# Performance work log

Hardware: AMD Instinct MI355X
Metric: run time of the kernel (lower is better)

## Reference

```python
import jax, jax.numpy as jnp
import numpy as np

B, T, D, H, E, NHEADS = 32, 512, 64, 128, 256, 8  # E = 2*H (bidirectional concat)


def setup_inputs() -> dict:
    key = jax.random.key(0)
    ks = jax.random.split(key, 20)
    s = 0.05

    def gl(k, shape):
        return jax.random.normal(k, shape, dtype=jnp.float32) * s

    inp = {}
    inp["x"] = jax.random.normal(ks[0], (B, T, D), dtype=jnp.float32)
    inp["mask"] = (jax.random.uniform(ks[1], (B, T, D)) > 0.3).astype(jnp.float32)
    # Fused GRU-D gate params per direction: rows ordered [r; z; n]
    inp["fwd_Wi"] = gl(ks[2], (3 * H, D));  inp["fwd_bi"] = gl(ks[3], (3 * H,))
    inp["fwd_Wh"] = gl(ks[4], (3 * H, H));  inp["fwd_bh"] = gl(ks[5], (3 * H,))
    inp["bwd_Wi"] = gl(ks[6], (3 * H, D));  inp["bwd_bi"] = gl(ks[7], (3 * H,))
    inp["bwd_Wh"] = gl(ks[8], (3 * H, H));  inp["bwd_bh"] = gl(ks[9], (3 * H,))
    # nn.MultiheadAttention params (in_proj packs q,k,v)
    inp["attn_w_in"] = gl(ks[10], (3 * E, E)); inp["attn_b_in"] = gl(ks[11], (3 * E,))
    inp["attn_w_out"] = gl(ks[12], (E, E));    inp["attn_b_out"] = gl(ks[13], (E,))
    # output projection 2H -> input_dim
    inp["out_w"] = gl(ks[14], (D, E));         inp["out_b"] = gl(ks[15], (D,))
    return inp


def gru_scan(xm, Wi, bi, Wh, bh):
    """GRU over time. xm: [T, B, D_in] (already mask-multiplied). Returns [T, B, H]."""
    Wh_rz, Wh_n = Wh[: 2 * H], Wh[2 * H :]
    bh_rz, bh_n = bh[: 2 * H], bh[2 * H :]

    def step(h, xt):
        gi = xt @ Wi.T + bi                      # [B, 3H]
        i_r, i_z, i_n = jnp.split(gi, 3, axis=-1)
        g_rz = h @ Wh_rz.T + bh_rz               # [B, 2H]
        r = jax.nn.sigmoid(i_r + g_rz[:, :H])
        z = jax.nn.sigmoid(i_z + g_rz[:, H:])
        n = jnp.tanh(i_n + (r * h) @ Wh_n.T + bh_n)
        h_new = (1.0 - z) * n + z * h
        return h_new, h_new

    h0 = jnp.zeros((xm.shape[1], H), dtype=xm.dtype)
    _, hs = jax.lax.scan(step, h0, xm)
    return hs


def mha(xt, Win, bin_, Wout, bout):
    """torch nn.MultiheadAttention (seq-first, self-attn, no mask). xt: [T, B, E]."""
    Tn, Bn, En = xt.shape
    hd = En // NHEADS
    qkv = xt @ Win.T + bin_                      # [T, B, 3E]
    q, k, v = jnp.split(qkv, 3, axis=-1)
    q = q.reshape(Tn, Bn, NHEADS, hd) * (1.0 / np.sqrt(hd))
    k = k.reshape(Tn, Bn, NHEADS, hd)
    v = v.reshape(Tn, Bn, NHEADS, hd)
    scores = jnp.einsum("tbhd,sbhd->bhts", q, k)   # [B, H, T, T]
    attn = jax.nn.softmax(scores, axis=-1)
    o = jnp.einsum("bhts,sbhd->tbhd", attn, v).reshape(Tn, Bn, En)
    return o @ Wout.T + bout


def reference(x, mask, fwd_Wi, fwd_bi, fwd_Wh, fwd_bh,
              bwd_Wi, bwd_bi, bwd_Wh, bwd_bh,
              attn_w_in, attn_b_in, attn_w_out, attn_b_out,
              out_w, out_b):
    xm = (x * mask).transpose(1, 0, 2)           # [T, B, D]
    hf = gru_scan(xm, fwd_Wi, fwd_bi, fwd_Wh, fwd_bh)                 # forward in time
    hb = gru_scan(xm[::-1], bwd_Wi, bwd_bi, bwd_Wh, bwd_bh)[::-1]     # backward in time
    hc = jnp.concatenate([hf, hb], axis=-1)      # [T, B, 2H]
    hc = mha(hc, attn_w_in, attn_b_in, attn_w_out, attn_b_out)
    imputed = (hc @ out_w.T + out_b).transpose(1, 0, 2)  # [B, T, D]
    output = x * mask + imputed * (1.0 - mask)
    return (output, imputed)
```

## Files before the change

kernel.cpp:

```cpp
#include <hip/hip_runtime.h>

#define TT 512
#define BB 32
#define DD 64
#define HH 128
#define EE 256
#define NR 16384

typedef _Float16 h2v __attribute__((ext_vector_type(2)));
typedef short bf16x8 __attribute__((ext_vector_type(8)));
typedef float f32x4 __attribute__((ext_vector_type(4)));

static __device__ __forceinline__ float bflo(unsigned u){ return __uint_as_float(u << 16); }
static __device__ __forceinline__ float bfhi(unsigned u){ return __uint_as_float(u & 0xFFFF0000u); }
static __device__ __forceinline__ unsigned short f2bf(float x){
  unsigned u = __float_as_uint(x);
  return (unsigned short)((u + 0x7FFFu + ((u >> 16) & 1u)) >> 16);
}
static __device__ __forceinline__ unsigned packbf(float a, float b){
  return (unsigned)f2bf(a) | ((unsigned)f2bf(b) << 16);
}
static __device__ __forceinline__ float sigmoidf_(float x){
  return 1.0f / (1.0f + __expf(-x));
}
static __device__ __forceinline__ float tanhf_(float x){
  float e = __expf(2.0f * x);
  return 1.0f - 2.0f / (e + 1.0f);
}
static __device__ __forceinline__ unsigned packh2(float a, float b){
  h2v v; v.x = (_Float16)a; v.y = (_Float16)b;
  return __builtin_bit_cast(unsigned, v);
}
#define BCH(u) __builtin_bit_cast(h2v, (u))
#define DOT2(a, b, c) __builtin_amdgcn_fdot2((a), (b), (c), false)
#define LGKM_BARRIER() asm volatile("s_waitcnt lgkmcnt(0)\n\ts_barrier" ::: "memory")

__global__ __launch_bounds__(256) void gi_mfma_kernel(
    const float* __restrict__ x, const float* __restrict__ mask,
    const float* __restrict__ WiF, const float* __restrict__ biF,
    const float* __restrict__ WiB, const float* __restrict__ biB,
    float* __restrict__ gi)
{
  __shared__ unsigned short As[64*72];
  __shared__ unsigned short Ws[64*72];
  int tid = threadIdx.x;
  int r0 = blockIdx.x * 64;
  int lane = tid & 63;
  int w = tid >> 6;
  int lr = lane & 15, lk = lane >> 4;

#pragma unroll
  for (int it = 0; it < 4; ++it) {
    int l = tid + it*256;
    int row = l >> 4, kq = l & 15;
    int r = r0 + row; int t = r >> 5, b = r & 31;
    const float* xr = x + ((size_t)b*TT + t)*DD + kq*4;
    const float* mr = mask + ((size_t)b*TT + t)*DD + kq*4;
    float4 xv = *(const float4*)xr;
    float4 mv = *(const float4*)mr;
    unsigned* dst = (unsigned*)&As[row*72 + kq*4];
    dst[0] = packbf(xv.x*mv.x, xv.y*mv.y);
    dst[1] = packbf(xv.z*mv.z, xv.w*mv.w);
  }

  for (int ch = 0; ch < 12; ++ch) {
    int c0 = ch * 64;
    __syncthreads();
#pragma unroll
    for (int it = 0; it < 4; ++it) {
      int l = tid + it*256;
      int col = l >> 4, kq = l & 15;
      int c = c0 + col;
      const float* wr = (c < 384 ? WiF + (size_t)c*64 : WiB + (size_t)(c-384)*64) + kq*4;
      float4 v = *(const float4*)wr;
      unsigned* dst = (unsigned*)&Ws[col*72 + kq*4];
      dst[0] = packbf(v.x, v.y);
      dst[1] = packbf(v.z, v.w);
    }
    __syncthreads();

    const unsigned short* arow = &As[(w*16 + lr)*72 + lk*8];
    f32x4 acc[4];
#pragma unroll
    for (int ct = 0; ct < 4; ++ct) {
      int cg = c0 + ct*16 + lr;
      float bv = (cg < 384) ? biF[cg] : biB[cg - 384];
      acc[ct][0] = bv; acc[ct][1] = bv; acc[ct][2] = bv; acc[ct][3] = bv;
    }
#pragma unroll
    for (int ks = 0; ks < 2; ++ks) {
      bf16x8 a = *(const bf16x8*)(arow + ks*32);
#pragma unroll
      for (int ct = 0; ct < 4; ++ct) {
        bf16x8 wv = *(const bf16x8*)&Ws[(ct*16 + lr)*72 + lk*8 + ks*32];
        acc[ct] = __builtin_amdgcn_mfma_f32_16x16x32_bf16(a, wv, acc[ct], 0, 0, 0);
      }
    }
#pragma unroll
    for (int ct = 0; ct < 4; ++ct) {
#pragma unroll
      for (int j = 0; j < 4; ++j) {
        int row = r0 + w*16 + lk*4 + j;
        gi[(size_t)row*768 + c0 + ct*16 + lr] = acc[ct][j];
      }
    }
  }
}

__global__ __launch_bounds__(256)
__attribute__((amdgpu_waves_per_eu(1, 1)))
void scan_kernel(
    const float* __restrict__ gi,
    const float* __restrict__ WhF, const float* __restrict__ bhF,
    const float* __restrict__ WhB, const float* __restrict__ bhB,
    float* __restrict__ hc)
{
  int dir = blockIdx.x >> 5;
  int b = blockIdx.x & 31;
  const float* Wh = dir ? WhB : WhF;
  const float* bh = dir ? bhB : bhF;
  int tid = threadIdx.x;
  int j2 = tid >> 1, h2 = tid & 1;

  __shared__ __align__(16) float h_s[128];
  __shared__ __align__(16) unsigned hs16[68];
  __shared__ __align__(16) unsigned rh16[76];
  __shared__ float z_s[128];

  const float* wp1 = Wh + (size_t)tid * 128;
#define LDA(n) unsigned A##n = packh2(wp1[2*(n)], wp1[2*(n)+1]);
  LDA(0) LDA(1) LDA(2) LDA(3) LDA(4) LDA(5) LDA(6) LDA(7)
  LDA(8) LDA(9) LDA(10) LDA(11) LDA(12) LDA(13) LDA(14) LDA(15)
  LDA(16) LDA(17) LDA(18) LDA(19) LDA(20) LDA(21) LDA(22) LDA(23)
  LDA(24) LDA(25) LDA(26) LDA(27) LDA(28) LDA(29) LDA(30) LDA(31)
  LDA(32) LDA(33) LDA(34) LDA(35) LDA(36) LDA(37) LDA(38) LDA(39)
  LDA(40) LDA(41) LDA(42) LDA(43) LDA(44) LDA(45) LDA(46) LDA(47)
  LDA(48) LDA(49) LDA(50) LDA(51) LDA(52) LDA(53) LDA(54) LDA(55)
  LDA(56) LDA(57) LDA(58) LDA(59) LDA(60) LDA(61) LDA(62) LDA(63)
#undef LDA
  const float* wp2 = Wh + (size_t)(256 + j2) * 128 + h2 * 64;
#define LDB(n) unsigned B##n = packh2(wp2[2*(n)], wp2[2*(n)+1]);
  LDB(0) LDB(1) LDB(2) LDB(3) LDB(4) LDB(5) LDB(6) LDB(7)
  LDB(8) LDB(9) LDB(10) LDB(11) LDB(12) LDB(13) LDB(14) LDB(15)
  LDB(16) LDB(17) LDB(18) LDB(19) LDB(20) LDB(21) LDB(22) LDB(23)
  LDB(24) LDB(25) LDB(26) LDB(27) LDB(28) LDB(29) LDB(30) LDB(31)
#undef LDB

  float bh1 = bh[tid];
  float bh2 = bh[256 + j2];

  if (tid < 128) h_s[tid] = 0.0f;
  if (tid < 68)  hs16[tid] = 0u;
  __syncthreads();

  size_t row0 = dir ? ((size_t)(TT-1)*BB + b) : (size_t)b;
  const float* grow = gi + row0 * 768 + dir * 384;
  long dstep = (dir ? -(long)BB : (long)BB) * 768;
  float gi1v = grow[tid];
  float gi2v = grow[256 + j2];

  for (int s = 0; s < TT; s++) {
#define PIN8(a,b_,c,d,e,f,g,hh) asm volatile("" : "+v"(a), "+v"(b_), "+v"(c), "+v"(d), "+v"(e), "+v"(f), "+v"(g), "+v"(hh));
    PIN8(A0,A1,A2,A3,A4,A5,A6,A7)
    PIN8(A8,A9,A10,A11,A12,A13,A14,A15)
    PIN8(A16,A17,A18,A19,A20,A21,A22,A23)
    PIN8(A24,A25,A26,A27,A28,A29,A30,A31)
    PIN8(A32,A33,A34,A35,A36,A37,A38,A39)
    PIN8(A40,A41,A42,A43,A44,A45,A46,A47)
    PIN8(A48,A49,A50,A51,A52,A53,A54,A55)
    PIN8(A56,A57,A58,A59,A60,A61,A62,A63)
    PIN8(B0,B1,B2,B3,B4,B5,B6,B7)
    PIN8(B8,B9,B10,B11,B12,B13,B14,B15)
    PIN8(B16,B17,B18,B19,B20,B21,B22,B23)
    PIN8(B24,B25,B26,B27,B28,B29,B30,B31)
#undef PIN8

    const float* gnext = grow + dstep;
    float gi1n = 0.f, gi2n = 0.f;
    if (s + 1 < TT) { gi1n = gnext[tid]; gi2n = gnext[256 + j2]; }

    float hold = h_s[tid & 127];

    const unsigned* hp0 = hs16;
    const unsigned* hp1 = hs16 + 36;
    float ya = 0.f, yb = 0.f, yc = 0.f, yd = 0.f;
#define S1(n, base, w0, w1, w2, w3) { uint4 hv = *(const uint4*)((base) + 4*(n)); \
    ya = DOT2(BCH(w0), BCH(hv.x), ya); yb = DOT2(BCH(w1), BCH(hv.y), yb); \
    yc = DOT2(BCH(w2), BCH(hv.z), yc); yd = DOT2(BCH(w3), BCH(hv.w), yd); }
    S1(0, hp0, A0,A1,A2,A3)     S1(1, hp0, A4,A5,A6,A7)
    S1(2, hp0, A8,A9,A10,A11)   S1(3, hp0, A12,A13,A14,A15)
    S1(4, hp0, A16,A17,A18,A19) S1(5, hp0, A20,A21,A22,A23)
    S1(6, hp0, A24,A25,A26,A27) S1(7, hp0, A28,A29,A30,A31)
    S1(0, hp1, A32,A33,A34,A35) S1(1, hp1, A36,A37,A38,A39)
    S1(2, hp1, A40,A41,A42,A43) S1(3, hp1, A44,A45,A46,A47)
    S1(4, hp1, A48,A49,A50,A51) S1(5, hp1, A52,A53,A54,A55)
    S1(6, hp1, A56,A57,A58,A59) S1(7, hp1, A60,A61,A62,A63)
#undef S1
    float y = (ya + yb) + (yc + yd);
    float sg = sigmoidf_(gi1v + y + bh1);
    float rhv = sg * hold;
    float rhp = __shfl_xor(rhv, 1);
    if (tid < 128) {
      if ((tid & 1) == 0) {
        int pi = tid >> 1;
        rh16[(pi & 15) + 20 * (pi >> 4)] = packh2(rhv, rhp);
      }
    } else {
      z_s[tid - 128] = sg;
    }
    LGKM_BARRIER();

    const unsigned* rp0 = rh16 + h2 * 40;
    const unsigned* rp1 = rp0 + 20;
    float ca = 0.f, cb = 0.f, cc = 0.f, cd = 0.f;
#define S2(n, base, w0, w1, w2, w3) { uint4 rv = *(const uint4*)((base) + 4*(n)); \
    ca = DOT2(BCH(w0), BCH(rv.x), ca); cb = DOT2(BCH(w1), BCH(rv.y), cb); \
    cc = DOT2(BCH(w2), BCH(rv.z), cc); cd = DOT2(BCH(w3), BCH(rv.w), cd); }
    S2(0, rp0, B0,B1,B2,B3)     S2(1, rp0, B4,B5,B6,B7)
    S2(2, rp0, B8,B9,B10,B11)   S2(3, rp0, B12,B13,B14,B15)
    S2(0, rp1, B16,B17,B18,B19) S2(1, rp1, B20,B21,B22,B23)
    S2(2, rp1, B24,B25,B26,B27) S2(3, rp1, B28,B29,B30,B31)
#undef S2
    float y2 = (ca + cb) + (cc + cd);
    y2 += __shfl_xor(y2, 1);
    float nn = tanhf_(gi2v + y2 + bh2);
    float zv = z_s[j2];
    float hv_ = h_s[j2];
    float hn = nn + zv * (hv_ - nn);
    float hnp = __shfl_xor(hn, 2);
    if (h2 == 0) {
      h_s[j2] = hn;
      int t = dir ? (TT - 1 - s) : s;
      hc[((size_t)t * BB + b) * EE + dir * HH + j2] = hn;
    }
    if ((tid & 3) == 0) {
      int pi = tid >> 2;
      hs16[(pi & 31) + 36 * (j2 >> 6)] = packh2(hn, hnp);
    }
    LGKM_BARRIER();
    gi1v = gi1n; gi2v = gi2n;
    grow = gnext;
  }
}

__global__ __launch_bounds__(256) void mfma_gemm_kernel(
    const float* __restrict__ A, const float* __restrict__ W,
    const float* __restrict__ bias, float* __restrict__ C,
    int N)
{
  __shared__ unsigned short As[64*264];
  __shared__ unsigned short Ws[64*264];
  int tid = threadIdx.x;
  int r0 = blockIdx.x * 64;
  int lane = tid & 63;
  int w = tid >> 6;
  int lr = lane & 15;
  int lk = lane >> 4;

#pragma unroll
  for (int it = 0; it < 16; ++it) {
    int l = tid + it*256;
    int row = l >> 6, kq = l & 63;
    float4 v = *(const float4*)(A + (size_t)(r0+row)*256 + kq*4);
    unsigned* dst = (unsigned*)&As[row*264 + kq*4];
    dst[0] = packbf(v.x, v.y);
    dst[1] = packbf(v.z, v.w);
  }

  const unsigned short* arow = &As[(w*16 + lr)*264 + lk*8];
  const unsigned short* wrow0 = &Ws[(0*16 + lr)*264 + lk*8];
  const unsigned short* wrow1 = &Ws[(1*16 + lr)*264 + lk*8];
  const unsigned short* wrow2 = &Ws[(2*16 + lr)*264 + lk*8];
  const unsigned short* wrow3 = &Ws[(3*16 + lr)*264 + lk*8];

  int nChunks = N >> 6;
  for (int ch = 0; ch < nChunks; ++ch) {
    int c0 = ch << 6;
    __syncthreads();
#pragma unroll
    for (int it = 0; it < 16; ++it) {
      int l = tid + it*256;
      int row = l >> 6, kq = l & 63;
      float4 v = *(const float4*)(W + (size_t)(c0+row)*256 + kq*4);
      unsigned* dst = (unsigned*)&Ws[row*264 + kq*4];
      dst[0] = packbf(v.x, v.y);
      dst[1] = packbf(v.z, v.w);
    }
    __syncthreads();

    float b0 = bias[c0 + lr], b1 = bias[c0 + 16 + lr];
    float b2 = bias[c0 + 32 + lr], b3 = bias[c0 + 48 + lr];
    f32x4 acc0 = {b0, b0, b0, b0};
    f32x4 acc1 = {b1, b1, b1, b1};
    f32x4 acc2 = {b2, b2, b2, b2};
    f32x4 acc3 = {b3, b3, b3, b3};

#pragma unroll
    for (int ks = 0; ks < 8; ++ks) {
      bf16x8 a  = *(const bf16x8*)(arow  + ks*32);
      bf16x8 q0 = *(const bf16x8*)(wrow0 + ks*32);
      bf16x8 q1 = *(const bf16x8*)(wrow1 + ks*32);
      bf16x8 q2 = *(const bf16x8*)(wrow2 + ks*32);
      bf16x8 q3 = *(const bf16x8*)(wrow3 + ks*32);
      acc0 = __builtin_amdgcn_mfma_f32_16x16x32_bf16(a, q0, acc0, 0, 0, 0);
      acc1 = __builtin_amdgcn_mfma_f32_16x16x32_bf16(a, q1, acc1, 0, 0, 0);
      acc2 = __builtin_amdgcn_mfma_f32_16x16x32_bf16(a, q2, acc2, 0, 0, 0);
      acc3 = __builtin_amdgcn_mfma_f32_16x16x32_bf16(a, q3, acc3, 0, 0, 0);
    }

#pragma unroll
    for (int j = 0; j < 4; ++j) {
      int row = r0 + w*16 + lk*4 + j;
      float* cp = C + (size_t)row * N + c0 + lr;
      cp[0]  = acc0[j];
      cp[16] = acc1[j];
      cp[32] = acc2[j];
      cp[48] = acc3[j];
    }
  }
}

__global__ __launch_bounds__(256, 1) void attn_mfma_kernel(
    const float* __restrict__ qkv, float* __restrict__ obuf)
{
  int b = blockIdx.x >> 3, h = blockIdx.x & 7;
  int tid = threadIdx.x;
  int lane = tid & 63;
  int w = tid >> 6;
  int lr = lane & 15, lk = lane >> 4;

  __shared__ unsigned short Ks[512*40];
  __shared__ unsigned short Vt[32*520];
  __shared__ unsigned short Sb[64*520];
  __shared__ unsigned short Qs[64*40];

  for (int l = tid; l < 4096; l += 256) {
    int s = l >> 3, dq = l & 7;
    const float* kr = qkv + ((size_t)s*BB + b)*768 + 256 + h*32 + dq*4;
    float4 kv = *(const float4*)kr;
    unsigned* kd = (unsigned*)&Ks[s*40 + dq*4];
    kd[0] = packbf(kv.x, kv.y);
    kd[1] = packbf(kv.z, kv.w);
    float4 vv = *(const float4*)(kr + 256);
    int sp = ((s & 15) << 5) + (s >> 4);
    Vt[(dq*4+0)*520 + sp] = f2bf(vv.x);
    Vt[(dq*4+1)*520 + sp] = f2bf(vv.y);
    Vt[(dq*4+2)*520 + sp] = f2bf(vv.z);
    Vt[(dq*4+3)*520 + sp] = f2bf(vv.w);
  }
  __syncthreads();

  const float SCL = 0.17677669529663687f;

  for (int p = 0; p < 8; ++p) {
    int q0 = p*64 + w*16;
#pragma unroll
    for (int i = 0; i < 2; ++i) {
      int l = lane + i*64;
      int row = l >> 3, dq = l & 7;
      const float* qr = qkv + ((size_t)(q0+row)*BB + b)*768 + h*32 + dq*4;
      float4 qv = *(const float4*)qr;
      unsigned* qd = (unsigned*)&Qs[(w*16+row)*40 + dq*4];
      qd[0] = packbf(qv.x*SCL, qv.y*SCL);
      qd[1] = packbf(qv.z*SCL, qv.w*SCL);
    }
    bf16x8 a = *(const bf16x8*)&Qs[(w*16+lr)*40 + lk*8];
    f32x4 st[32];
#pragma unroll
    for (int t = 0; t < 32; ++t) {
      bf16x8 kb = *(const bf16x8*)&Ks[(t*16+lr)*40 + lk*8];
      f32x4 z = {0.f, 0.f, 0.f, 0.f};
      st[t] = __builtin_amdgcn_mfma_f32_16x16x32_bf16(a, kb, z, 0, 0, 0);
    }
    float inv[4];
#pragma unroll
    for (int j = 0; j < 4; ++j) {
      float m = -3e38f;
#pragma unroll
      for (int t = 0; t < 32; ++t) m = fmaxf(m, st[t][j]);
      m = fmaxf(m, __shfl_xor(m, 1));
      m = fmaxf(m, __shfl_xor(m, 2));
      m = fmaxf(m, __shfl_xor(m, 4));
      m = fmaxf(m, __shfl_xor(m, 8));
      float sum = 0.f;
#pragma unroll
      for (int t = 0; t < 32; ++t) { float e = __expf(st[t][j] - m); st[t][j] = e; sum += e; }
      sum += __shfl_xor(sum, 1);
      sum += __shfl_xor(sum, 2);
      sum += __shfl_xor(sum, 4);
      sum += __shfl_xor(sum, 8);
      inv[j] = 1.0f / sum;
    }
#pragma unroll
    for (int j = 0; j < 4; ++j) {
      unsigned pk[16];
#pragma unroll
      for (int i = 0; i < 16; ++i)
        pk[i] = packbf(st[2*i][j]*inv[j], st[2*i+1][j]*inv[j]);
      uint4* dst = (uint4*)&Sb[(w*16 + lk*4 + j)*520 + lr*32];
      dst[0] = make_uint4(pk[0], pk[1], pk[2], pk[3]);
      dst[1] = make_uint4(pk[4], pk[5], pk[6], pk[7]);
      dst[2] = make_uint4(pk[8], pk[9], pk[10], pk[11]);
      dst[3] = make_uint4(pk[12], pk[13], pk[14], pk[15]);
    }
    f32x4 o0 = {0.f,0.f,0.f,0.f}, o1 = {0.f,0.f,0.f,0.f};
#pragma unroll
    for (int kt = 0; kt < 16; ++kt) {
      bf16x8 pa = *(const bf16x8*)&Sb[(w*16 + lr)*520 + kt*32 + lk*8];
      bf16x8 v0 = *(const bf16x8*)&Vt[(lr)*520 + kt*32 + lk*8];
      bf16x8 v1 = *(const bf16x8*)&Vt[(16 + lr)*520 + kt*32 + lk*8];
      o0 = __builtin_amdgcn_mfma_f32_16x16x32_bf16(pa, v0, o0, 0, 0, 0);
      o1 = __builtin_amdgcn_mfma_f32_16x16x32_bf16(pa, v1, o1, 0, 0, 0);
    }
#pragma unroll
    for (int j = 0; j < 4; ++j) {
      int q = q0 + lk*4 + j;
      float* op = obuf + ((size_t)q*BB + b)*EE + h*32;
      op[lr]      = o0[j];
      op[16 + lr] = o1[j];
    }
  }
}

__global__ __launch_bounds__(256) void fuse_w_kernel(
    const float* __restrict__ aWout, const float* __restrict__ about,
    const float* __restrict__ oW, const float* __restrict__ ob,
    float* __restrict__ Wf, float* __restrict__ bf)
{
  int g = blockIdx.x;
  int k = threadIdx.x;
  const float* owr = oW + (size_t)g * 256;
  float acc = 0.f;
  for (int j = 0; j < 256; ++j)
    acc += owr[j] * aWout[(size_t)j * 256 + k];
  Wf[(size_t)g * 256 + k] = acc;
  if (k == 0) {
    float a = ob[g];
    for (int j = 0; j < 256; ++j) a += owr[j] * about[j];
    bf[g] = a;
  }
}

__global__ __launch_bounds__(256) void final_kernel(
    const float* __restrict__ A,
    const float* __restrict__ W,
    const float* __restrict__ bias,
    const float* __restrict__ x, const float* __restrict__ mask,
    float* __restrict__ out)
{
  __shared__ float As[64*260];
  __shared__ unsigned Ws[64*130];
  int tid = threadIdx.x;
  int ty = tid >> 4, tx = tid & 15;
  int r0 = blockIdx.x * 64;

  for (int l = tid; l < 4096; l += 256) {
    int row = l >> 6, kq = l & 63;
    float4 v = *(const float4*)(A + (size_t)(r0 + row)*256 + kq*4);
    *(float4*)&As[row*260 + kq*4] = v;
  }
  for (int l = tid; l < 4096; l += 256) {
    int c = l >> 6, kq = l & 63;
    float4 v = *(const float4*)(W + (size_t)c*256 + kq*4);
    uint2 p; p.x = packbf(v.x, v.y); p.y = packbf(v.z, v.w);
    *(uint2*)&Ws[c*130 + kq*2] = p;
  }
  __syncthreads();

  float acc[4][4];
#pragma unroll
  for (int rj = 0; rj < 4; rj++)
#pragma unroll
    for (int cj = 0; cj < 4; cj++)
      acc[rj][cj] = bias[tx + 16*cj];

#pragma unroll 2
  for (int kq = 0; kq < 64; kq++) {
    float4 av[4];
#pragma unroll
    for (int rj = 0; rj < 4; rj++)
      av[rj] = *(const float4*)&As[(ty*4+rj)*260 + 4*kq];
#pragma unroll
    for (int cj = 0; cj < 4; cj++) {
      uint2 w2 = *(const uint2*)&Ws[(tx + 16*cj)*130 + 2*kq];
      float w0 = bflo(w2.x), w1 = bfhi(w2.x);
      float w2f = bflo(w2.y), w3 = bfhi(w2.y);
#pragma unroll
      for (int rj = 0; rj < 4; rj++)
        acc[rj][cj] += av[rj].x*w0 + av[rj].y*w1 + av[rj].z*w2f + av[rj].w*w3;
    }
  }

#pragma unroll
  for (int rj = 0; rj < 4; rj++) {
    int r = r0 + ty*4 + rj;
    int t = r >> 5, b = r & 31;
    size_t base = ((size_t)b * TT + t) * DD;
#pragma unroll
    for (int cj = 0; cj < 4; cj++) {
      int c = tx + 16*cj;
      float imp = acc[rj][cj];
      float xv = x[base + c], mv = mask[base + c];
      out[base + c] = xv*mv + imp*(1.0f - mv);
      out[(size_t)1048576 + base + c] = imp;
    }
  }
}

extern "C" void kernel_launch(void* const* d_in, const int* in_sizes, int n_in,
                              void* d_out, int out_size, void* d_ws, size_t ws_size,
                              hipStream_t stream) {
  const float* x     = (const float*)d_in[0];
  const float* mask  = (const float*)d_in[1];
  const float* fWi   = (const float*)d_in[2];
  const float* fbi   = (const float*)d_in[3];
  const float* fWh   = (const float*)d_in[4];
  const float* fbh   = (const float*)d_in[5];
  const float* bWi   = (const float*)d_in[6];
  const float* bbi   = (const float*)d_in[7];
  const float* bWh   = (const float*)d_in[8];
  const float* bbh   = (const float*)d_in[9];
  const float* aWin  = (const float*)d_in[10];
  const float* abin  = (const float*)d_in[11];
  const float* aWout = (const float*)d_in[12];
  const float* about = (const float*)d_in[13];
  const float* oW    = (const float*)d_in[14];
  const float* ob    = (const float*)d_in[15];
  float* out = (float*)d_out;
  float* ws  = (float*)d_ws;

  float* gi   = ws;
  float* hc   = ws + 12582912;
  float* qkv  = ws;
  float* obuf = ws + 12582912;
  float* Wf   = ws;
  float* bf   = ws + 16384;

  gi_mfma_kernel<<<256, 256, 0, stream>>>(x, mask, fWi, fbi, bWi, bbi, gi);
  scan_kernel<<<64, 256, 0, stream>>>(gi, fWh, fbh, bWh, bbh, hc);
  mfma_gemm_kernel<<<256, 256, 0, stream>>>(hc, aWin, abin, qkv, 768);
  attn_mfma_kernel<<<256, 256, 0, stream>>>(qkv, obuf);
  fuse_w_kernel<<<64, 256, 0, stream>>>(aWout, about, oW, ob, Wf, bf);
  final_kernel<<<256, 256, 0, stream>>>(obuf, Wf, bf, x, mask, out);
}
```

Measured before the change: 599.9 us.

## Batch GRU recurrence across 16 sequences per block using bf16 MFMA

The recurrent scan now has each block handle 16 batch rows for one direction and computes the hidden-state matmuls with bf16 MFMA instructions, using register-resident weight fragments. This replaces the previous design of one block per sequence using fp16 dot2 instructions. The grid shrinks from 64 blocks to 4, so far fewer CUs are used, but each step does 16x the work per block on matrix cores. Precision moves from fp16 to bf16 for the recurrent state, which may increase accumulated error over the 512 steps.

```diff
diff --git a/kernel.cpp b/kernel.cpp
--- a/kernel.cpp
+++ b/kernel.cpp
@@ -7,7 +7,6 @@
 #define EE 256
 #define NR 16384
 
-typedef _Float16 h2v __attribute__((ext_vector_type(2)));
 typedef short bf16x8 __attribute__((ext_vector_type(8)));
 typedef float f32x4 __attribute__((ext_vector_type(4)));
 
@@ -27,13 +26,16 @@
   float e = __expf(2.0f * x);
   return 1.0f - 2.0f / (e + 1.0f);
 }
-static __device__ __forceinline__ unsigned packh2(float a, float b){
-  h2v v; v.x = (_Float16)a; v.y = (_Float16)b;
-  return __builtin_bit_cast(unsigned, v);
-}
-#define BCH(u) __builtin_bit_cast(h2v, (u))
-#define DOT2(a, b, c) __builtin_amdgcn_fdot2((a), (b), (c), false)
 #define LGKM_BARRIER() asm volatile("s_waitcnt lgkmcnt(0)\n\ts_barrier" ::: "memory")
+
+static __device__ __forceinline__ bf16x8 ldwfrag(const float* p){
+  float4 u = *(const float4*)p;
+  float4 v = *(const float4*)(p + 4);
+  uint4 q;
+  q.x = packbf(u.x, u.y); q.y = packbf(u.z, u.w);
+  q.z = packbf(v.x, v.y); q.w = packbf(v.z, v.w);
+  return __builtin_bit_cast(bf16x8, q);
+}
 
 __global__ __launch_bounds__(256) void gi_mfma_kernel(
     const float* __restrict__ x, const float* __restrict__ mask,
@@ -109,136 +111,165 @@
 
 __global__ __launch_bounds__(256)
 __attribute__((amdgpu_waves_per_eu(1, 1)))
-void scan_kernel(
+void scan_mfma_kernel(
     const float* __restrict__ gi,
     const float* __restrict__ WhF, const float* __restrict__ bhF,
     const float* __restrict__ WhB, const float* __restrict__ bhB,
     float* __restrict__ hc)
 {
-  int dir = blockIdx.x >> 5;
-  int b = blockIdx.x & 31;
+  int dir = blockIdx.x >> 1;
+  int bhalf = blockIdx.x & 1;
   const float* Wh = dir ? WhB : WhF;
   const float* bh = dir ? bhB : bhF;
   int tid = threadIdx.x;
-  int j2 = tid >> 1, h2 = tid & 1;
-
-  __shared__ __align__(16) float h_s[128];
-  __shared__ __align__(16) unsigned hs16[68];
-  __shared__ __align__(16) unsigned rh16[76];
-  __shared__ float z_s[128];
-
-  const float* wp1 = Wh + (size_t)tid * 128;
-#define LDA(n) unsigned A##n = packh2(wp1[2*(n)], wp1[2*(n)+1]);
-  LDA(0) LDA(1) LDA(2) LDA(3) LDA(4) LDA(5) LDA(6) LDA(7)
-  LDA(8) LDA(9) LDA(10) LDA(11) LDA(12) LDA(13) LDA(14) LDA(15)
-  LDA(16) LDA(17) LDA(18) LDA(19) LDA(20) LDA(21) LDA(22) LDA(23)
-  LDA(24) LDA(25) LDA(26) LDA(27) LDA(28) LDA(29) LDA(30) LDA(31)
-  LDA(32) LDA(33) LDA(34) LDA(35) LDA(36) LDA(37) LDA(38) LDA(39)
-  LDA(40) LDA(41) LDA(42) LDA(43) LDA(44) LDA(45) LDA(46) LDA(47)
-  LDA(48) LDA(49) LDA(50) LDA(51) LDA(52) LDA(53) LDA(54) LDA(55)
-  LDA(56) LDA(57) LDA(58) LDA(59) LDA(60) LDA(61) LDA(62) LDA(63)
-#undef LDA
-  const float* wp2 = Wh + (size_t)(256 + j2) * 128 + h2 * 64;
-#define LDB(n) unsigned B##n = packh2(wp2[2*(n)], wp2[2*(n)+1]);
-  LDB(0) LDB(1) LDB(2) LDB(3) LDB(4) LDB(5) LDB(6) LDB(7)
-  LDB(8) LDB(9) LDB(10) LDB(11) LDB(12) LDB(13) LDB(14) LDB(15)
-  LDB(16) LDB(17) LDB(18) LDB(19) LDB(20) LDB(21) LDB(22) LDB(23)
-  LDB(24) LDB(25) LDB(26) LDB(27) LDB(28) LDB(29) LDB(30) LDB(31)
-#undef LDB
-
-  float bh1 = bh[tid];
-  float bh2 = bh[256 + j2];
-
-  if (tid < 128) h_s[tid] = 0.0f;
-  if (tid < 68)  hs16[tid] = 0u;
+  int lane = tid & 63;
+  int w = tid >> 6;
+  int lr = lane & 15, lk = lane >> 4;
+
+  __shared__ unsigned short h16[16*136];
+  __shared__ unsigned short rh16[16*136];
+  __shared__ float hf[16*132];
+  __shared__ float zf[16*132];
+
+  bf16x8 WB1[4][4];
+#pragma unroll
+  for (int ct = 0; ct < 4; ++ct)
+#pragma unroll
+    for (int ks = 0; ks < 4; ++ks)
+      WB1[ct][ks] = ldwfrag(Wh + (size_t)((w*4+ct)*16 + lr)*128 + ks*32 + lk*8);
+  bf16x8 WB2[2][4];
+#pragma unroll
+  for (int ti = 0; ti < 2; ++ti)
+#pragma unroll
+    for (int ks = 0; ks < 4; ++ks)
+      WB2[ti][ks] = ldwfrag(Wh + (size_t)(256 + w*32 + ti*16 + lr)*128 + ks*32 + lk*8);
+
+  float bh1[4], bh2[2];
+#pragma unroll
+  for (int ct = 0; ct < 4; ++ct) bh1[ct] = bh[(w*4+ct)*16 + lr];
+#pragma unroll
+  for (int ti = 0; ti < 2; ++ti) bh2[ti] = bh[256 + w*32 + ti*16 + lr];
+
+  for (int l = tid; l < 16*136; l += 256) { h16[l] = 0; rh16[l] = 0; }
+  for (int l = tid; l < 16*132; l += 256) { hf[l] = 0.0f; zf[l] = 0.0f; }
   __syncthreads();
 
-  size_t row0 = dir ? ((size_t)(TT-1)*BB + b) : (size_t)b;
-  const float* grow = gi + row0 * 768 + dir * 384;
   long dstep = (dir ? -(long)BB : (long)BB) * 768;
-  float gi1v = grow[tid];
-  float gi2v = grow[256 + j2];
-
-  for (int s = 0; s < TT; s++) {
-#define PIN8(a,b_,c,d,e,f,g,hh) asm volatile("" : "+v"(a), "+v"(b_), "+v"(c), "+v"(d), "+v"(e), "+v"(f), "+v"(g), "+v"(hh));
-    PIN8(A0,A1,A2,A3,A4,A5,A6,A7)
-    PIN8(A8,A9,A10,A11,A12,A13,A14,A15)
-    PIN8(A16,A17,A18,A19,A20,A21,A22,A23)
-    PIN8(A24,A25,A26,A27,A28,A29,A30,A31)
-    PIN8(A32,A33,A34,A35,A36,A37,A38,A39)
-    PIN8(A40,A41,A42,A43,A44,A45,A46,A47)
-    PIN8(A48,A49,A50,A51,A52,A53,A54,A55)
-    PIN8(A56,A57,A58,A59,A60,A61,A62,A63)
-    PIN8(B0,B1,B2,B3,B4,B5,B6,B7)
-    PIN8(B8,B9,B10,B11,B12,B13,B14,B15)
-    PIN8(B16,B17,B18,B19,B20,B21,B22,B23)
-    PIN8(B24,B25,B26,B27,B28,B29,B30,B31)
-#undef PIN8
-
+  int t0_ = dir ? (TT-1) : 0;
+  const float* grow = gi + (size_t)(t0_*BB + bhalf*16) * 768 + dir*384;
+
+  float g1[4][4], g2[2][4];
+#pragma unroll
+  for (int ct = 0; ct < 4; ++ct)
+#pragma unroll
+    for (int j = 0; j < 4; ++j)
+      g1[ct][j] = grow[(size_t)(lk*4+j)*768 + (w*4+ct)*16 + lr];
+#pragma unroll
+  for (int ti = 0; ti < 2; ++ti)
+#pragma unroll
+    for (int j = 0; j < 4; ++j)
+      g2[ti][j] = grow[(size_t)(lk*4+j)*768 + 256 + w*32 + ti*16 + lr];
+
+  for (int s = 0; s < TT; ++s) {
+    int t = dir ? (TT - 1 - s) : s;
     const float* gnext = grow + dstep;
-    float gi1n = 0.f, gi2n = 0.f;
-    if (s + 1 < TT) { gi1n = gnext[tid]; gi2n = gnext[256 + j2]; }
-
-    float hold = h_s[tid & 127];
-
-    const unsigned* hp0 = hs16;
-    const unsigned* hp1 = hs16 + 36;
-    float ya = 0.f, yb = 0.f, yc = 0.f, yd = 0.f;
-#define S1(n, base, w0, w1, w2, w3) { uint4 hv = *(const uint4*)((base) + 4*(n)); \
-    ya = DOT2(BCH(w0), BCH(hv.x), ya); yb = DOT2(BCH(w1), BCH(hv.y), yb); \
-    yc = DOT2(BCH(w2), BCH(hv.z), yc); yd = DOT2(BCH(w3), BCH(hv.w), yd); }
-    S1(0, hp0, A0,A1,A2,A3)     S1(1, hp0, A4,A5,A6,A7)
-    S1(2, hp0, A8,A9,A10,A11)   S1(3, hp0, A12,A13,A14,A15)
-    S1(4, hp0, A16,A17,A18,A19) S1(5, hp0, A20,A21,A22,A23)
-    S1(6, hp0, A24,A25,A26,A27) S1(7, hp0, A28,A29,A30,A31)
-    S1(0, hp1, A32,A33,A34,A35) S1(1, hp1, A36,A37,A38,A39)
-    S1(2, hp1, A40,A41,A42,A43) S1(3, hp1, A44,A45,A46,A47)
-    S1(4, hp1, A48,A49,A50,A51) S1(5, hp1, A52,A53,A54,A55)
-    S1(6, hp1, A56,A57,A58,A59) S1(7, hp1, A60,A61,A62,A63)
-#undef S1
-    float y = (ya + yb) + (yc + yd);
-    float sg = sigmoidf_(gi1v + y + bh1);
-    float rhv = sg * hold;
-    float rhp = __shfl_xor(rhv, 1);
-    if (tid < 128) {
-      if ((tid & 1) == 0) {
-        int pi = tid >> 1;
-        rh16[(pi & 15) + 20 * (pi >> 4)] = packh2(rhv, rhp);
+
+    float g1n[4][4], g2n[2][4];
+    if (s + 1 < TT) {
+#pragma unroll
+      for (int ct = 0; ct < 4; ++ct)
+#pragma unroll
+        for (int j = 0; j < 4; ++j)
+          g1n[ct][j] = gnext[(size_t)(lk*4+j)*768 + (w*4+ct)*16 + lr];
+#pragma unroll
+      for (int ti = 0; ti < 2; ++ti)
+#pragma unroll
+        for (int j = 0; j < 4; ++j)
+          g2n[ti][j] = gnext[(size_t)(lk*4+j)*768 + 256 + w*32 + ti*16 + lr];
+    } else {
+#pragma unroll
+      for (int ct = 0; ct < 4; ++ct)
+#pragma unroll
+        for (int j = 0; j < 4; ++j) g1n[ct][j] = 0.f;
+#pragma unroll
+      for (int ti = 0; ti < 2; ++ti)
+#pragma unroll
+        for (int j = 0; j < 4; ++j) g2n[ti][j] = 0.f;
+    }
+
+    bf16x8 af[4];
+#pragma unroll
+    for (int ks = 0; ks < 4; ++ks)
+      af[ks] = *(const bf16x8*)&h16[lr*136 + ks*32 + lk*8];
+
+#pragma unroll
+    for (int ct = 0; ct < 4; ++ct) {
+      f32x4 acc;
+      acc[0] = g1[ct][0] + bh1[ct];
+      acc[1] = g1[ct][1] + bh1[ct];
+      acc[2] = g1[ct][2] + bh1[ct];
+      acc[3] = g1[ct][3] + bh1[ct];
+#pragma unroll
+      for (int ks = 0; ks < 4; ++ks)
+        acc = __builtin_amdgcn_mfma_f32_16x16x32_bf16(af[ks], WB1[ct][ks], acc, 0, 0, 0);
+      if (w < 2) {
+#pragma unroll
+        for (int j = 0; j < 4; ++j) {
+          int row = lk*4 + j;
+          int col = w*64 + ct*16 + lr;
+          float rv = sigmoidf_(acc[j]);
+          float ho = hf[row*132 + col];
+          rh16[row*136 + col] = f2bf(rv * ho);
+        }
+      } else {
+#pragma unroll
+        for (int j = 0; j < 4; ++j) {
+          int row = lk*4 + j;
+          int col = (w-2)*64 + ct*16 + lr;
+          zf[row*132 + col] = sigmoidf_(acc[j]);
+        }
       }
-    } else {
-      z_s[tid - 128] = sg;
     }
     LGKM_BARRIER();
 
-    const unsigned* rp0 = rh16 + h2 * 40;
-    const unsigned* rp1 = rp0 + 20;
-    float ca = 0.f, cb = 0.f, cc = 0.f, cd = 0.f;
-#define S2(n, base, w0, w1, w2, w3) { uint4 rv = *(const uint4*)((base) + 4*(n)); \
-    ca = DOT2(BCH(w0), BCH(rv.x), ca); cb = DOT2(BCH(w1), BCH(rv.y), cb); \
-    cc = DOT2(BCH(w2), BCH(rv.z), cc); cd = DOT2(BCH(w3), BCH(rv.w), cd); }
-    S2(0, rp0, B0,B1,B2,B3)     S2(1, rp0, B4,B5,B6,B7)
-    S2(2, rp0, B8,B9,B10,B11)   S2(3, rp0, B12,B13,B14,B15)
-    S2(0, rp1, B16,B17,B18,B19) S2(1, rp1, B20,B21,B22,B23)
-    S2(2, rp1, B24,B25,B26,B27) S2(3, rp1, B28,B29,B30,B31)
-#undef S2
-    float y2 = (ca + cb) + (cc + cd);
-    y2 += __shfl_xor(y2, 1);
-    float nn = tanhf_(gi2v + y2 + bh2);
-    float zv = z_s[j2];
-    float hv_ = h_s[j2];
-    float hn = nn + zv * (hv_ - nn);
-    float hnp = __shfl_xor(hn, 2);
-    if (h2 == 0) {
-      h_s[j2] = hn;
-      int t = dir ? (TT - 1 - s) : s;
-      hc[((size_t)t * BB + b) * EE + dir * HH + j2] = hn;
-    }
-    if ((tid & 3) == 0) {
-      int pi = tid >> 2;
-      hs16[(pi & 31) + 36 * (j2 >> 6)] = packh2(hn, hnp);
+    bf16x8 ar[4];
+#pragma unroll
+    for (int ks = 0; ks < 4; ++ks)
+      ar[ks] = *(const bf16x8*)&rh16[lr*136 + ks*32 + lk*8];
+
+#pragma unroll
+    for (int ti = 0; ti < 2; ++ti) {
+      f32x4 acc;
+      acc[0] = g2[ti][0] + bh2[ti];
+      acc[1] = g2[ti][1] + bh2[ti];
+      acc[2] = g2[ti][2] + bh2[ti];
+      acc[3] = g2[ti][3] + bh2[ti];
+#pragma unroll
+      for (int ks = 0; ks < 4; ++ks)
+        acc = __builtin_amdgcn_mfma_f32_16x16x32_bf16(ar[ks], WB2[ti][ks], acc, 0, 0, 0);
+#pragma unroll
+      for (int j = 0; j < 4; ++j) {
+        int row = lk*4 + j;
+        int col = w*32 + ti*16 + lr;
+        float nn = tanhf_(acc[j]);
+        float zv = zf[row*132 + col];
+        float ho = hf[row*132 + col];
+        float hn = nn + zv * (ho - nn);
+        hf[row*132 + col] = hn;
+        h16[row*136 + col] = f2bf(hn);
+        hc[((size_t)t*BB + bhalf*16 + row) * EE + dir*HH + col] = hn;
+      }
     }
     LGKM_BARRIER();
-    gi1v = gi1n; gi2v = gi2n;
+
+#pragma unroll
+    for (int ct = 0; ct < 4; ++ct)
+#pragma unroll
+      for (int j = 0; j < 4; ++j) g1[ct][j] = g1n[ct][j];
+#pragma unroll
+    for (int ti = 0; ti < 2; ++ti)
+#pragma unroll
+      for (int j = 0; j < 4; ++j) g2[ti][j] = g2n[ti][j];
     grow = gnext;
   }
 }
@@ -537,7 +568,7 @@
   float* bf   = ws + 16384;
 
   gi_mfma_kernel<<<256, 256, 0, stream>>>(x, mask, fWi, fbi, bWi, bbi, gi);
-  scan_kernel<<<64, 256, 0, stream>>>(gi, fWh, fbh, bWh, bbh, hc);
+  scan_mfma_kernel<<<4, 256, 0, stream>>>(gi, fWh, fbh, bWh, bbh, hc);
   mfma_gemm_kernel<<<256, 256, 0, stream>>>(hc, aWin, abin, qkv, 768);
   attn_mfma_kernel<<<256, 256, 0, stream>>>(qkv, obuf);
   fuse_w_kernel<<<64, 256, 0, stream>>>(aWout, about, oW, ob, Wf, bf);
```

After: 1.424 ms. 137% more time.
